# Kernel tuning notes

Hardware: AMD Instinct MI355X
Metric: run time of the kernel (lower is better)

Reference implementation:

```python
import jax, jax.numpy as jnp
import numpy as np

N = 100000      # nodes
E = 1250000     # edges
DIN = 64        # input_dim
H = 64          # hidden_dim
G = 64          # graphs in batch


def setup_inputs() -> dict:
    key = jax.random.key(0)
    ks = jax.random.split(key, 12)
    s = lambda d: 1.0 / np.sqrt(d)  # glorot-ish scale
    return {
        "x": jax.random.normal(ks[0], (N, DIN), dtype=jnp.float32),
        "W1": jax.random.normal(ks[1], (DIN, H), dtype=jnp.float32) * s(DIN),
        "b1": jnp.zeros((H,), jnp.float32),
        "W2": jax.random.normal(ks[2], (H, H), dtype=jnp.float32) * s(H),
        "b2": jnp.zeros((H,), jnp.float32),
        "W3": jax.random.normal(ks[3], (H, H), dtype=jnp.float32) * s(H),
        "b3": jnp.zeros((H,), jnp.float32),
        "Wc1": jax.random.normal(ks[4], (H, H // 2), dtype=jnp.float32) * s(H),
        "bc1": jnp.zeros((H // 2,), jnp.float32),
        "Wc2": jax.random.normal(ks[5], (H // 2, 2), dtype=jnp.float32) * s(H // 2),
        "bc2": jnp.zeros((2,), jnp.float32),
        "edge_index": jax.random.randint(ks[6], (2, E), 0, N, dtype=jnp.int64),
        "batch": jnp.sort(jax.random.randint(ks[7], (N,), 0, G, dtype=jnp.int64)),
    }


def _gcn_norm(edge_index, num_nodes):
    # add self loops, compute symmetric normalization coefficients
    loop = jnp.arange(num_nodes, dtype=edge_index.dtype)
    src = jnp.concatenate([edge_index[0], loop])
    dst = jnp.concatenate([edge_index[1], loop])
    deg = jax.ops.segment_sum(jnp.ones_like(dst, dtype=jnp.float32), dst,
                              num_segments=num_nodes)
    dinv = jnp.where(deg > 0, jax.lax.rsqrt(deg), 0.0)
    norm = dinv[src] * dinv[dst]  # [E+N]
    return src, dst, norm


def _gcn_conv(x, src, dst, norm, W, b, num_nodes):
    h = x @ W                              # [N, out]
    msgs = h[src] * norm[:, None]          # gather + scale, [E+N, out]
    agg = jax.ops.segment_sum(msgs, dst, num_segments=num_nodes)
    return agg + b


def reference(x, W1, b1, W2, b2, W3, b3, Wc1, bc1, Wc2, bc2, edge_index, batch):
    num_nodes = x.shape[0]
    src, dst, norm = _gcn_norm(edge_index, num_nodes)
    h = jax.nn.relu(_gcn_conv(x, src, dst, norm, W1, b1, num_nodes))
    h = jax.nn.relu(_gcn_conv(h, src, dst, norm, W2, b2, num_nodes))
    h = jax.nn.relu(_gcn_conv(h, src, dst, norm, W3, b3, num_nodes))
    # global mean pool over graphs
    sums = jax.ops.segment_sum(h, batch, num_segments=G)          # [G, H]
    cnts = jax.ops.segment_sum(jnp.ones_like(batch, dtype=h.dtype), batch,
                               num_segments=G)
    pooled = sums / jnp.maximum(cnts, 1.0)[:, None]
    # classifier MLP (dropout inactive at inference)
    z = jax.nn.relu(pooled @ Wc1 + bc1)
    return z @ Wc2 + bc2                                          # [G, 2]
```

## Files before the change

### kernel.cpp

```cpp
#include <hip/hip_runtime.h>

constexpr int N = 100000;
constexpr int E = 1250000;
constexpr int G = 64;
constexpr int K = 32;
constexpr int OVF_CAP = 65536;
constexpr int STRIPES = 8;
constexpr int NPS = N / STRIPES;
constexpr int SCAP = 164 * 1024;
constexpr int PR = 1024;
constexpr int PROUNDS = 2;
constexpr int PCHUNK = PR * PROUNDS;
constexpr int PBLKS = (E + PCHUNK - 1) / PCHUNK;
constexpr int SUBN = 391;
constexpr int SUBS = 32;
constexpr int SCAP2 = 6 * 1024;
constexpr int P2CAP = 240;

typedef int v4i __attribute__((ext_vector_type(4)));

__device__ inline unsigned bf16pack(float a, float b) {
  unsigned ua = __float_as_uint(a);
  ua = (ua + 0x7FFF + ((ua >> 16) & 1)) >> 16;
  unsigned ub = __float_as_uint(b);
  ub = (ub + 0x7FFF + ((ub >> 16) & 1)) & 0xFFFF0000u;
  return ua | ub;
}

__global__ void part_kernel(const int* __restrict__ src, const int* __restrict__ dst,
                            unsigned* __restrict__ staged, int* __restrict__ cursors) {
  __shared__ unsigned bins[STRIPES][PR];
  __shared__ int bcnt[STRIPES];
  __shared__ int bbase[STRIPES];
  int tid = threadIdx.x;
  if (tid < STRIPES) bcnt[tid] = 0;
  __syncthreads();
  int base0 = blockIdx.x * PCHUNK;
  auto bin1 = [&](int s, int d) {
    int st = d / NPS;
    unsigned w = ((unsigned)s << 14) | (unsigned)(d - st * NPS);
    int p = atomicAdd(&bcnt[st], 1);
    bins[st][p] = w;
  };
#pragma unroll 1
  for (int r = 0; r < PROUNDS; r++) {
    int base = base0 + r * PR + tid * 4;
    if (base + 3 < E) {
      v4i s4 = __builtin_nontemporal_load((const v4i*)(src + base));
      v4i d4 = __builtin_nontemporal_load((const v4i*)(dst + base));
      bin1(s4.x, d4.x); bin1(s4.y, d4.y); bin1(s4.z, d4.z); bin1(s4.w, d4.w);
    } else {
      for (int j = 0; j < 4; j++)
        if (base + j < E) bin1(src[base + j], dst[base + j]);
    }
    __syncthreads();
    if (tid < STRIPES) bbase[tid] = atomicAdd(&cursors[tid], bcnt[tid]);
    __syncthreads();
#pragma unroll 1
    for (int b = 0; b < STRIPES; b++) {
      int c = bcnt[b];
      unsigned* out = staged + (size_t)b * SCAP + bbase[b];
      for (int k = tid; k < c; k += 256) out[k] = bins[b][k];
    }
    __syncthreads();
    if (tid < STRIPES) bcnt[tid] = 0;
    __syncthreads();
  }
}

__global__ void part2_kernel(const unsigned* __restrict__ staged, const int* __restrict__ cursors,
                             unsigned* __restrict__ staged2, int* __restrict__ cursors2,
                             float* __restrict__ sums) {
  __shared__ unsigned bins[SUBS][P2CAP];
  __shared__ int bcnt[SUBS];
  __shared__ int bbase[SUBS];
  int tid = threadIdx.x;
  if (blockIdx.x == 0) {
    for (int i = tid; i < G * 64 + G; i += 256) sums[i] = 0.f;
  }
  int s = blockIdx.x & (STRIPES - 1);
  int blk = blockIdx.x >> 3;
  if (tid < SUBS) bcnt[tid] = 0;
  __syncthreads();
  int n = cursors[s];
  const unsigned* sbuf = staged + (size_t)s * SCAP;
  int chunk = (n + SUBS - 1) / SUBS;
  int lo2 = blk * chunk, hi2 = min(lo2 + chunk, n);
  for (int i = lo2 + tid; i < hi2; i += 256) {
    unsigned w = __builtin_nontemporal_load(sbuf + i);
    int local = (int)(w & 0x3FFFu);
    int b = local / SUBN;
    int slot = atomicAdd(&bcnt[b], 1);
    if (slot < P2CAP) {
      bins[b][slot] = w;
    } else {
      int q = atomicAdd(&cursors2[s * SUBS + b], 1);
      staged2[(size_t)(s * SUBS + b) * SCAP2 + q] = w;
    }
  }
  __syncthreads();
  if (tid < SUBS) bbase[tid] = atomicAdd(&cursors2[s * SUBS + tid], min(bcnt[tid], P2CAP));
  __syncthreads();
#pragma unroll 1
  for (int b = 0; b < SUBS; b++) {
    int c = min(bcnt[b], P2CAP);
    unsigned* out = staged2 + (size_t)(s * SUBS + b) * SCAP2 + bbase[b];
    for (int k = tid; k < c; k += 256) out[k] = bins[b][k];
  }
}

__global__ __launch_bounds__(512)
void fill_kernel(const unsigned* __restrict__ staged2, const int* __restrict__ cursors2,
                 int* __restrict__ cnt, int* __restrict__ csr,
                 int* __restrict__ ovf, int* __restrict__ ovf_cnt) {
  __shared__ int lcnt[SUBN];
  __shared__ int lcsr[SUBN * K];
  int strp = blockIdx.x & (STRIPES - 1);
  int sub = blockIdx.x >> 3;
  int tid = threadIdx.x;
  for (int i = tid; i < SUBN; i += 512) lcnt[i] = 0;
  __syncthreads();
  int idx2 = strp * SUBS + sub;
  int n2 = cursors2[idx2];
  const unsigned* sbuf = staged2 + (size_t)idx2 * SCAP2;
  int lo = sub * SUBN;
  int nodes = min(SUBN, NPS - lo);
  for (int i = tid; i < n2; i += 512) {
    unsigned w = sbuf[i];
    int local = (int)(w & 0x3FFFu);
    int ld = local - lo;
    int slot = atomicAdd(&lcnt[ld], 1);
    int sr = (int)(w >> 14);
    if (slot < K) {
      lcsr[ld * K + slot] = sr;
    } else {
      int q = atomicAdd(ovf_cnt, 1);
      if (q < OVF_CAP) { ovf[2 * q] = sr; ovf[2 * q + 1] = strp * NPS + local; }
    }
  }
  __syncthreads();
  int nb = strp * NPS + lo;
  for (int i = tid; i < nodes; i += 512) cnt[nb + i] = lcnt[i];
  uint4* dstp = (uint4*)(csr + (size_t)nb * K);
  const uint4* srcp = (const uint4*)lcsr;
  int q4 = nodes * (K / 4);
  for (int i = tid; i < q4; i += 512) dstp[i] = srcp[i];
}

constexpr int XS_STRIDE = 68;
__global__ void gemm_premul_kernel(const float* __restrict__ X, const float* __restrict__ W,
                                   const int* __restrict__ cnt, unsigned* __restrict__ Hs2) {
  __shared__ float Ws[64 * 64];
  __shared__ float Xs[32 * XS_STRIDE];
  int tid = threadIdx.x;
  const float4* W4 = (const float4*)W;
#pragma unroll
  for (int j = 0; j < 4; j++)
    ((float4*)Ws)[tid + j * 256] = W4[tid + j * 256];
  int row0 = blockIdx.x * 32;
  const float4* X4 = (const float4*)(X + row0 * 64);
#pragma unroll
  for (int j = 0; j < 2; j++) {
    int idx = tid + j * 256;
    int r = idx >> 4, q = idx & 15;
    *((float4*)&Xs[r * XS_STRIDE + q * 4]) = X4[idx];
  }
  __syncthreads();
  int r0 = tid >> 4;
  int c = (tid & 15) * 4;
  float4 acc0 = {0, 0, 0, 0}, acc1 = {0, 0, 0, 0};
#pragma unroll
  for (int k = 0; k < 64; k++) {
    float4 w = *((const float4*)&Ws[k * 64 + c]);
    float xa = Xs[r0 * XS_STRIDE + k];
    float xb = Xs[(r0 + 16) * XS_STRIDE + k];
    acc0.x += xa * w.x; acc0.y += xa * w.y; acc0.z += xa * w.z; acc0.w += xa * w.w;
    acc1.x += xb * w.x; acc1.y += xb * w.y; acc1.z += xb * w.z; acc1.w += xb * w.w;
  }
  int ra = row0 + r0, rb = ra + 16;
  float da = rsqrtf((float)cnt[ra] + 1.0f);
  float db = rsqrtf((float)cnt[rb] + 1.0f);
  uint2 pa = make_uint2(bf16pack(acc0.x * da, acc0.y * da), bf16pack(acc0.z * da, acc0.w * da));
  uint2 pb = make_uint2(bf16pack(acc1.x * db, acc1.y * db), bf16pack(acc1.z * db, acc1.w * db));
  ((uint2*)Hs2)[ra * 16 + (tid & 15)] = pa;
  ((uint2*)Hs2)[rb * 16 + (tid & 15)] = pb;
}

template <bool LAST>
__global__ void agg_kernel(const unsigned* __restrict__ Hs2, const int* __restrict__ cnt,
                           const int* __restrict__ csr, const int* __restrict__ ovf,
                           const int* __restrict__ ovf_cnt, const float* __restrict__ b,
                           float* __restrict__ Xout, const int* __restrict__ batch,
                           float* __restrict__ sums, float* __restrict__ cnts) {
  __shared__ float gsum[4][64];
  __shared__ float gcnt[4];
  __shared__ int gmin_s;
  int tid = threadIdx.x;
  if constexpr (LAST) {
    if (tid < 256) {
      ((float*)gsum)[tid] = 0.f;
      if (tid < 4) gcnt[tid] = 0.f;
      if (tid == 0) gmin_s = batch[blockIdx.x * 32];
    }
    __syncthreads();
  }
  int lane = tid & 63;
  int i = lane & 7;
  int gb = lane & 56;
  int node = blockIdx.x * 32 + (tid >> 3);
  int c = cnt[node];
  int mg = min(c, K);
  int sv0 = csr[node * K + i];
  int sv1 = csr[node * K + 8 + i];
  int sv2 = csr[node * K + 16 + i];
  int sv3 = csr[node * K + 24 + i];
  int mm = mg;
  mm = max(mm, __shfl_xor(mm, 8));
  mm = max(mm, __shfl_xor(mm, 16));
  mm = max(mm, __shfl_xor(mm, 32));
  const uint4* H4 = (const uint4*)Hs2;
  float acc0 = 0, acc1 = 0, acc2 = 0, acc3 = 0, acc4 = 0, acc5 = 0, acc6 = 0, acc7 = 0;
  auto accm = [&](uint4 h, float m) {
    acc0 = fmaf(m, __uint_as_float(h.x << 16), acc0);
    acc1 = fmaf(m, __uint_as_float(h.x & 0xFFFF0000u), acc1);
    acc2 = fmaf(m, __uint_as_float(h.y << 16), acc2);
    acc3 = fmaf(m, __uint_as_float(h.y & 0xFFFF0000u), acc3);
    acc4 = fmaf(m, __uint_as_float(h.z << 16), acc4);
    acc5 = fmaf(m, __uint_as_float(h.z & 0xFFFF0000u), acc5);
    acc6 = fmaf(m, __uint_as_float(h.w << 16), acc6);
    acc7 = fmaf(m, __uint_as_float(h.w & 0xFFFF0000u), acc7);
  };
  auto edge8 = [&](int sv, int eb) {
    int t0 = __shfl(sv, gb + 0), t1 = __shfl(sv, gb + 1);
    int t2 = __shfl(sv, gb + 2), t3 = __shfl(sv, gb + 3);
    int t4 = __shfl(sv, gb + 4), t5 = __shfl(sv, gb + 5);
    int t6 = __shfl(sv, gb + 6), t7 = __shfl(sv, gb + 7);
    uint4 h0 = H4[(size_t)(eb + 0 < mg ? t0 : node) * 8 + i];
    uint4 h1 = H4[(size_t)(eb + 1 < mg ? t1 : node) * 8 + i];
    uint4 h2 = H4[(size_t)(eb + 2 < mg ? t2 : node) * 8 + i];
    uint4 h3 = H4[(size_t)(eb + 3 < mg ? t3 : node) * 8 + i];
    uint4 h4 = H4[(size_t)(eb + 4 < mg ? t4 : node) * 8 + i];
    uint4 h5 = H4[(size_t)(eb + 5 < mg ? t5 : node) * 8 + i];
    uint4 h6 = H4[(size_t)(eb + 6 < mg ? t6 : node) * 8 + i];
    uint4 h7 = H4[(size_t)(eb + 7 < mg ? t7 : node) * 8 + i];
    accm(h0, eb + 0 < mg ? 1.f : 0.f);
    accm(h1, eb + 1 < mg ? 1.f : 0.f);
    accm(h2, eb + 2 < mg ? 1.f : 0.f);
    accm(h3, eb + 3 < mg ? 1.f : 0.f);
    accm(h4, eb + 4 < mg ? 1.f : 0.f);
    accm(h5, eb + 5 < mg ? 1.f : 0.f);
    accm(h6, eb + 6 < mg ? 1.f : 0.f);
    accm(h7, eb + 7 < mg ? 1.f : 0.f);
  };
  if (mm > 0)  edge8(sv0, 0);
  if (mm > 8)  edge8(sv1, 8);
  if (mm > 16) edge8(sv2, 16);
  if (mm > 24) edge8(sv3, 24);
  int on = min(*ovf_cnt, OVF_CAP);
  for (int j = 0; j < on; j++) {
    int dd = ovf[2 * j + 1];
    if (dd == node) {
      uint4 h = H4[(size_t)ovf[2 * j] * 8 + i];
      accm(h, 1.f);
    }
  }
  uint4 hs = H4[(size_t)node * 8 + i];
  float di = rsqrtf((float)c + 1.0f);
  const float4* b4 = (const float4*)b;
  float4 blo = b4[2 * i], bhi = b4[2 * i + 1];
  float4 o0, o1;
  o0.x = fmaxf(di * (acc0 + __uint_as_float(hs.x << 16)) + blo.x, 0.f);
  o0.y = fmaxf(di * (acc1 + __uint_as_float(hs.x & 0xFFFF0000u)) + blo.y, 0.f);
  o0.z = fmaxf(di * (acc2 + __uint_as_float(hs.y << 16)) + blo.z, 0.f);
  o0.w = fmaxf(di * (acc3 + __uint_as_float(hs.y & 0xFFFF0000u)) + blo.w, 0.f);
  o1.x = fmaxf(di * (acc4 + __uint_as_float(hs.z << 16)) + bhi.x, 0.f);
  o1.y = fmaxf(di * (acc5 + __uint_as_float(hs.z & 0xFFFF0000u)) + bhi.y, 0.f);
  o1.z = fmaxf(di * (acc6 + __uint_as_float(hs.w << 16)) + bhi.z, 0.f);
  o1.w = fmaxf(di * (acc7 + __uint_as_float(hs.w & 0xFFFF0000u)) + bhi.w, 0.f);
  if constexpr (!LAST) {
    ((float4*)Xout)[node * 16 + 2 * i] = o0;
    ((float4*)Xout)[node * 16 + 2 * i + 1] = o1;
  } else {
    int g = batch[node];
    int ref = __shfl(g, i);
    if (__all(g == ref)) {
      float v0 = o0.x, v1 = o0.y, v2 = o0.z, v3 = o0.w;
      float v4 = o1.x, v5 = o1.y, v6 = o1.z, v7 = o1.w;
#pragma unroll
      for (int off = 8; off < 64; off <<= 1) {
        v0 += __shfl_xor(v0, off); v1 += __shfl_xor(v1, off);
        v2 += __shfl_xor(v2, off); v3 += __shfl_xor(v3, off);
        v4 += __shfl_xor(v4, off); v5 += __shfl_xor(v5, off);
        v6 += __shfl_xor(v6, off); v7 += __shfl_xor(v7, off);
      }
      if (gb == 0) {
        int s = ref - gmin_s;
        atomicAdd(&gsum[s][8 * i + 0], v0); atomicAdd(&gsum[s][8 * i + 1], v1);
        atomicAdd(&gsum[s][8 * i + 2], v2); atomicAdd(&gsum[s][8 * i + 3], v3);
        atomicAdd(&gsum[s][8 * i + 4], v4); atomicAdd(&gsum[s][8 * i + 5], v5);
        atomicAdd(&gsum[s][8 * i + 6], v6); atomicAdd(&gsum[s][8 * i + 7], v7);
        if (i == 0) atomicAdd(&gcnt[s], 8.f);
      }
    } else {
      int s = g - gmin_s;
      if ((unsigned)s < 4u) {
        atomicAdd(&gsum[s][8 * i + 0], o0.x); atomicAdd(&gsum[s][8 * i + 1], o0.y);
        atomicAdd(&gsum[s][8 * i + 2], o0.z); atomicAdd(&gsum[s][8 * i + 3], o0.w);
        atomicAdd(&gsum[s][8 * i + 4], o1.x); atomicAdd(&gsum[s][8 * i + 5], o1.y);
        atomicAdd(&gsum[s][8 * i + 6], o1.z); atomicAdd(&gsum[s][8 * i + 7], o1.w);
        if (i == 0) atomicAdd(&gcnt[s], 1.f);
      } else {
        atomicAdd(&sums[g * 64 + 8 * i + 0], o0.x); atomicAdd(&sums[g * 64 + 8 * i + 1], o0.y);
        atomicAdd(&sums[g * 64 + 8 * i + 2], o0.z); atomicAdd(&sums[g * 64 + 8 * i + 3], o0.w);
        atomicAdd(&sums[g * 64 + 8 * i + 4], o1.x); atomicAdd(&sums[g * 64 + 8 * i + 5], o1.y);
        atomicAdd(&sums[g * 64 + 8 * i + 6], o1.z); atomicAdd(&sums[g * 64 + 8 * i + 7], o1.w);
        if (i == 0) atomicAdd(&cnts[g], 1.f);
      }
    }
    __syncthreads();
    if (tid < 256) {
      int s2 = tid >> 6, d = tid & 63;
      if (gcnt[s2] > 0.f) {
        atomicAdd(&sums[(gmin_s + s2) * 64 + d], gsum[s2][d]);
        if (d == 0) atomicAdd(&cnts[gmin_s + s2], gcnt[s2]);
      }
    }
  }
}

__global__ void classifier_kernel(const float* __restrict__ sums, const float* __restrict__ cnts,
                                  const float* __restrict__ Wc1, const float* __restrict__ bc1,
                                  const float* __restrict__ Wc2, const float* __restrict__ bc2,
                                  float* __restrict__ out) {
  __shared__ float pooled[64 * 64];
  __shared__ float z[64 * 32];
  int tid = threadIdx.x;
  for (int idx = tid; idx < 64 * 64; idx += 256) {
    int g = idx >> 6;
    pooled[idx] = sums[idx] / fmaxf(cnts[g], 1.0f);
  }
  __syncthreads();
  for (int idx = tid; idx < 64 * 32; idx += 256) {
    int g = idx >> 5, j = idx & 31;
    float acc = bc1[j];
#pragma unroll
    for (int c = 0; c < 64; c++) acc += pooled[g * 64 + c] * Wc1[c * 32 + j];
    z[idx] = fmaxf(acc, 0.f);
  }
  __syncthreads();
  for (int idx = tid; idx < 128; idx += 256) {
    int g = idx >> 1, k = idx & 1;
    float acc = bc2[k];
#pragma unroll
    for (int j = 0; j < 32; j++) acc += z[g * 32 + j] * Wc2[j * 2 + k];
    out[idx] = acc;
  }
}

extern "C" void kernel_launch(void* const* d_in, const int* in_sizes, int n_in,
                              void* d_out, int out_size, void* d_ws, size_t ws_size,
                              hipStream_t stream) {
  const float* x   = (const float*)d_in[0];
  const float* W1  = (const float*)d_in[1];
  const float* b1  = (const float*)d_in[2];
  const float* W2  = (const float*)d_in[3];
  const float* b2  = (const float*)d_in[4];
  const float* W3  = (const float*)d_in[5];
  const float* b3  = (const float*)d_in[6];
  const float* Wc1 = (const float*)d_in[7];
  const float* bc1 = (const float*)d_in[8];
  const float* Wc2 = (const float*)d_in[9];
  const float* bc2 = (const float*)d_in[10];
  const int* ei    = (const int*)d_in[11];
  const int* batch = (const int*)d_in[12];
  const int* src  = ei;
  const int* dstp = ei + E;

  char* ws = (char*)d_ws;
  size_t off = 0;
  auto alloc = [&](size_t bytes) {
    char* p = ws + off;
    off += (bytes + 255) & ~size_t(255);
    return p;
  };
  int*      cnt  = (int*)alloc((size_t)(N + 512) * 4);
  int*      csr  = (int*)alloc((size_t)N * K * 4);
  int*      ovf  = (int*)alloc((size_t)OVF_CAP * 2 * 4);
  unsigned* Hs   = (unsigned*)alloc((size_t)N * 64 * 2);
  float*    B1   = (float*)alloc((size_t)N * 64 * 4);
  float*    sums = (float*)alloc((size_t)(G * 64 + G) * 4);
  float*    cnts = sums + G * 64;
  int*      ovf_cnt  = cnt + N;
  int*      cursors  = cnt + N + 16;
  int*      cursors2 = cnt + N + 64;
  unsigned* staged  = (unsigned*)B1;
  unsigned* staged2 = (unsigned*)B1 + (size_t)STRIPES * SCAP;

  hipMemsetAsync(cnt + N, 0, 512 * 4, stream);

  part_kernel<<<PBLKS, 256, 0, stream>>>(src, dstp, staged, cursors);
  part2_kernel<<<STRIPES * SUBS, 256, 0, stream>>>(staged, cursors, staged2, cursors2, sums);
  fill_kernel<<<STRIPES * SUBS, 512, 0, stream>>>(staged2, cursors2, cnt, csr, ovf, ovf_cnt);

  const float* Xc = x;
  const float* Wl[3] = {W1, W2, W3};
  const float* bl[3] = {b1, b2, b3};
  for (int l = 0; l < 3; l++) {
    gemm_premul_kernel<<<N / 32, 256, 0, stream>>>(Xc, Wl[l], cnt, Hs);
    if (l < 2)
      agg_kernel<false><<<N / 32, 256, 0, stream>>>(Hs, cnt, csr, ovf, ovf_cnt, bl[l], B1,
                                                    batch, sums, cnts);
    else
      agg_kernel<true><<<N / 32, 256, 0, stream>>>(Hs, cnt, csr, ovf, ovf_cnt, bl[l], B1,
                                                   batch, sums, cnts);
    Xc = B1;
  }

  classifier_kernel<<<1, 256, 0, stream>>>(sums, cnts, Wc1, bc1, Wc2, bc2, (float*)d_out);
}
```

Baseline: 280.2 us.

## Fuse next layer's GEMM into the aggregation kernel epilogue

The aggregation kernel for layers 1 and 2 now loads the next layer's weight matrix into shared memory. It multiplies each block's 32 aggregated rows by that matrix, scales by the degree factor, and writes bf16 pre-scaled features directly. This removes two separate GEMM launches and the fp32 round trip of the intermediate activations through global memory, and ping-pongs between two bf16 feature buffers. In exchange, the kernel takes on extra shared memory (about 25 KB), a block-wide sync, and per-thread FMA work in the epilogue, which may reduce occupancy for the gather phase.

```diff
diff --git a/kernel.cpp b/kernel.cpp
--- a/kernel.cpp
+++ b/kernel.cpp
@@ -187,21 +187,29 @@
 }
 
 template <bool LAST>
-__global__ void agg_kernel(const unsigned* __restrict__ Hs2, const int* __restrict__ cnt,
-                           const int* __restrict__ csr, const int* __restrict__ ovf,
-                           const int* __restrict__ ovf_cnt, const float* __restrict__ b,
-                           float* __restrict__ Xout, const int* __restrict__ batch,
-                           float* __restrict__ sums, float* __restrict__ cnts) {
-  __shared__ float gsum[4][64];
-  __shared__ float gcnt[4];
+__global__ __launch_bounds__(256)
+void agg_kernel(const unsigned* __restrict__ Hs2, const int* __restrict__ cnt,
+                const int* __restrict__ csr, const int* __restrict__ ovf,
+                const int* __restrict__ ovf_cnt, const float* __restrict__ b,
+                const float* __restrict__ Wn, unsigned* __restrict__ HsN,
+                const int* __restrict__ batch,
+                float* __restrict__ sums, float* __restrict__ cnts) {
+  __shared__ float smem[64 * 64 + 32 * 68];
   __shared__ int gmin_s;
-  int tid = threadIdx.x;
-  if constexpr (LAST) {
-    if (tid < 256) {
-      ((float*)gsum)[tid] = 0.f;
-      if (tid < 4) gcnt[tid] = 0.f;
-      if (tid == 0) gmin_s = batch[blockIdx.x * 32];
-    }
+  float* WLds = smem;
+  float (*rowLds)[68] = (float(*)[68])(smem + 4096);
+  float (*gsum)[64] = (float(*)[64])smem;
+  float* gcnt = smem + 256;
+  int tid = threadIdx.x;
+  if constexpr (!LAST) {
+    const float4* W4 = (const float4*)Wn;
+#pragma unroll
+    for (int j = 0; j < 4; j++)
+      ((float4*)WLds)[tid + j * 256] = W4[tid + j * 256];
+  } else {
+    smem[tid] = 0.f;
+    if (tid < 4) gcnt[tid] = 0.f;
+    if (tid == 0) gmin_s = batch[blockIdx.x * 32];
     __syncthreads();
   }
   int lane = tid & 63;
@@ -259,10 +267,7 @@
   int on = min(*ovf_cnt, OVF_CAP);
   for (int j = 0; j < on; j++) {
     int dd = ovf[2 * j + 1];
-    if (dd == node) {
-      uint4 h = H4[(size_t)ovf[2 * j] * 8 + i];
-      accm(h, 1.f);
-    }
+    if (dd == node) accm(H4[(size_t)ovf[2 * j] * 8 + i], 1.f);
   }
   uint4 hs = H4[(size_t)node * 8 + i];
   float di = rsqrtf((float)c + 1.0f);
@@ -278,8 +283,29 @@
   o1.z = fmaxf(di * (acc6 + __uint_as_float(hs.w << 16)) + bhi.z, 0.f);
   o1.w = fmaxf(di * (acc7 + __uint_as_float(hs.w & 0xFFFF0000u)) + bhi.w, 0.f);
   if constexpr (!LAST) {
-    ((float4*)Xout)[node * 16 + 2 * i] = o0;
-    ((float4*)Xout)[node * 16 + 2 * i + 1] = o1;
+    int n32 = tid >> 3;
+    *(float4*)&rowLds[n32][8 * i] = o0;
+    *(float4*)&rowLds[n32][8 * i + 4] = o1;
+    __syncthreads();
+    int r = tid >> 3;
+    int cq = (tid & 7) * 2;
+    float a0 = 0, a1 = 0, a2 = 0, a3 = 0, a4 = 0, a5 = 0, a6 = 0, a7 = 0;
+#pragma unroll
+    for (int k = 0; k < 64; k++) {
+      float xv = rowLds[r][k];
+      const float4* wr = (const float4*)(WLds + k * 64);
+      float4 w0 = wr[cq], w1 = wr[cq + 1];
+      a0 = fmaf(xv, w0.x, a0); a1 = fmaf(xv, w0.y, a1);
+      a2 = fmaf(xv, w0.z, a2); a3 = fmaf(xv, w0.w, a3);
+      a4 = fmaf(xv, w1.x, a4); a5 = fmaf(xv, w1.y, a5);
+      a6 = fmaf(xv, w1.z, a6); a7 = fmaf(xv, w1.w, a7);
+    }
+    uint4 p;
+    p.x = bf16pack(a0 * di, a1 * di);
+    p.y = bf16pack(a2 * di, a3 * di);
+    p.z = bf16pack(a4 * di, a5 * di);
+    p.w = bf16pack(a6 * di, a7 * di);
+    ((uint4*)HsN)[(size_t)node * 8 + (tid & 7)] = p;
   } else {
     int g = batch[node];
     int ref = __shfl(g, i);
@@ -386,7 +412,8 @@
   int*      cnt  = (int*)alloc((size_t)(N + 512) * 4);
   int*      csr  = (int*)alloc((size_t)N * K * 4);
   int*      ovf  = (int*)alloc((size_t)OVF_CAP * 2 * 4);
-  unsigned* Hs   = (unsigned*)alloc((size_t)N * 64 * 2);
+  unsigned* HsA  = (unsigned*)alloc((size_t)N * 64 * 2);
+  unsigned* HsB  = (unsigned*)alloc((size_t)N * 64 * 2);
   float*    B1   = (float*)alloc((size_t)N * 64 * 4);
   float*    sums = (float*)alloc((size_t)(G * 64 + G) * 4);
   float*    cnts = sums + G * 64;
@@ -402,19 +429,13 @@
   part2_kernel<<<STRIPES * SUBS, 256, 0, stream>>>(staged, cursors, staged2, cursors2, sums);
   fill_kernel<<<STRIPES * SUBS, 512, 0, stream>>>(staged2, cursors2, cnt, csr, ovf, ovf_cnt);
 
-  const float* Xc = x;
-  const float* Wl[3] = {W1, W2, W3};
-  const float* bl[3] = {b1, b2, b3};
-  for (int l = 0; l < 3; l++) {
-    gemm_premul_kernel<<<N / 32, 256, 0, stream>>>(Xc, Wl[l], cnt, Hs);
-    if (l < 2)
-      agg_kernel<false><<<N / 32, 256, 0, stream>>>(Hs, cnt, csr, ovf, ovf_cnt, bl[l], B1,
-                                                    batch, sums, cnts);
-    else
-      agg_kernel<true><<<N / 32, 256, 0, stream>>>(Hs, cnt, csr, ovf, ovf_cnt, bl[l], B1,
-                                                   batch, sums, cnts);
-    Xc = B1;
-  }
+  gemm_premul_kernel<<<N / 32, 256, 0, stream>>>(x, W1, cnt, HsA);
+  agg_kernel<false><<<N / 32, 256, 0, stream>>>(HsA, cnt, csr, ovf, ovf_cnt, b1,
+                                                W2, HsB, batch, sums, cnts);
+  agg_kernel<false><<<N / 32, 256, 0, stream>>>(HsB, cnt, csr, ovf, ovf_cnt, b2,
+                                                W3, HsA, batch, sums, cnts);
+  agg_kernel<true><<<N / 32, 256, 0, stream>>>(HsA, cnt, csr, ovf, ovf_cnt, b3,
+                                               W1, HsB, batch, sums, cnts);
 
   classifier_kernel<<<1, 256, 0, stream>>>(sums, cnts, Wc1, bc1, Wc2, bc2, (float*)d_out);
 }
```

After: 256.9 us. -8.3%, faster.
